# Optimization experiments

Hardware: AMD Instinct MI355X
Metric: run time of the kernel (lower is better)

## Reference

```python
import jax, jax.numpy as jnp
import numpy as np

B, N, D = 1, 2048, 512        # batch, query seq len, model dim
H, DH = 8, 64                 # heads, head dim
MEM = 512                     # cached XL memory tokens (one window segment)
KV = N + MEM                  # kv sequence length
WINDOW = 512                  # block / sliding-window size
LOOKBACK = 1                  # lookback_blocks
N_EP = 4                      # number of episodes
SCALE = DH ** -0.5


def _rope(t, pos):
    # t: [b,h,l,dh], pos: [l]  (GPT-NeoX half rotation)
    dh = t.shape[-1]
    inv_freq = 1.0 / (10000.0 ** (jnp.arange(0, dh, 2, dtype=jnp.float32) / dh))
    freqs = pos.astype(jnp.float32)[:, None] * inv_freq[None, :]   # [l, dh/2]
    freqs = jnp.concatenate([freqs, freqs], axis=-1)               # [l, dh]
    cos, sin = jnp.cos(freqs), jnp.sin(freqs)
    x1, x2 = jnp.split(t, 2, axis=-1)
    rotated = jnp.concatenate([-x2, x1], axis=-1)
    return t * cos + rotated * sin


def setup_inputs() -> dict:
    key = jax.random.key(0)
    ks = jax.random.split(key, 8)
    x = jax.random.normal(ks[0], (B, N, D), jnp.float32)
    cache_k = jax.random.normal(ks[1], (B, H, MEM, DH), jnp.float32)
    cache_v = jax.random.normal(ks[2], (B, H, MEM, DH), jnp.float32)
    episode_ids = jnp.sort(jax.random.randint(ks[3], (B, KV), 0, N_EP, dtype=jnp.int32), axis=-1)
    Wq = jax.random.normal(ks[4], (D, H * DH), jnp.float32) * 0.02
    Wkv = jax.random.normal(ks[5], (D, 2 * H * DH), jnp.float32) * 0.02
    Wg = jax.random.normal(ks[6], (D, H), jnp.float32) * 0.02
    Wo = jax.random.normal(ks[7], (H * DH, D), jnp.float32) * 0.02
    return dict(x=x, cache_k=cache_k, cache_v=cache_v, episode_ids=episode_ids,
                Wq=Wq, Wkv=Wkv, Wg=Wg, Wo=Wo)


def _xl_mask(episode_ids):
    # mirrors create_xl_mask: causal + block window with lookback + intra-episode
    offset = KV - N
    q_pos = offset + jnp.arange(N)          # [N]
    k_pos = jnp.arange(KV)                  # [KV]
    causal = q_pos[:, None] >= k_pos[None, :]
    bq = q_pos // WINDOW
    bk = k_pos // WINDOW
    block = (bq[:, None] >= bk[None, :]) & (bq[:, None] <= bk[None, :] + LOOKBACK)
    intra_ep = episode_ids[:, q_pos][:, :, None] == episode_ids[:, None, :]  # [B,N,KV]
    return (causal & block)[None] & intra_ep                                 # [B,N,KV]


def reference(x, cache_k, cache_v, episode_ids, Wq, Wkv, Wg, Wo):
    b, n, _ = x.shape
    offset = KV - N

    q = (x @ Wq).reshape(b, n, H, DH).transpose(0, 2, 1, 3)          # [b,h,n,dh]
    kv = (x @ Wkv).reshape(b, n, 2, H, DH)
    k_new = kv[:, :, 0].transpose(0, 2, 1, 3)                        # [b,h,n,dh]
    v_new = kv[:, :, 1].transpose(0, 2, 1, 3)

    k = jnp.concatenate([cache_k, k_new], axis=2)                    # [b,h,kv,dh]
    v = jnp.concatenate([cache_v, v_new], axis=2)

    q = _rope(q, offset + jnp.arange(n))
    k = _rope(k, jnp.arange(KV))

    scores = jnp.einsum('bhnd,bhmd->bhnm', q, k) * SCALE             # [b,h,n,kv]
    mask = _xl_mask(episode_ids)[:, None]                            # [b,1,n,kv]
    scores = jnp.where(mask, scores, jnp.finfo(scores.dtype).min)
    attn = jax.nn.softmax(scores, axis=-1)

    out = jnp.einsum('bhnm,bhmd->bhnd', attn, v)                     # [b,h,n,dh]

    gates = jax.nn.sigmoid(x @ Wg).transpose(0, 2, 1)[..., None]     # [b,h,n,1]
    out = out * gates

    out = out.transpose(0, 2, 1, 3).reshape(b, n, H * DH)            # merge heads
    return out @ Wo                                                  # [b,n,d]
```

## Files before the change

kernel.cpp:

```cpp
#include <hip/hip_runtime.h>
#include <math.h>

#define NQ     2048
#define DMODEL 512
#define NH     8
#define DHD    64
#define MEMT   512
#define KVT    2560
#define QSCALE 0.125f
#define NEGF   (-1e30f)

typedef unsigned short u16;
typedef __bf16 bf16x8 __attribute__((ext_vector_type(8)));
typedef float  f32x4  __attribute__((ext_vector_type(4)));
typedef u16    u16x8  __attribute__((ext_vector_type(8)));
typedef u16    u16x4  __attribute__((ext_vector_type(4)));

__device__ __forceinline__ u16 f2bf(float f) {
    union { float f; unsigned u; } v; v.f = f;
    unsigned r = (v.u + 0x7FFFu + ((v.u >> 16) & 1u)) >> 16;
    return (u16)r;
}

__global__ __launch_bounds__(256) void prep(const float* __restrict__ x,
                                            const float* __restrict__ Wq,
                                            const float* __restrict__ Wkv,
                                            const float* __restrict__ Wo,
                                            u16* __restrict__ xb,
                                            u16* __restrict__ Wt,
                                            u16* __restrict__ Wot) {
    __shared__ float tile[64][65];
    int bx = blockIdx.x, tid = threadIdx.x;
    if (bx < 64) {
        int base4 = bx * 4096;
#pragma unroll
        for (int u = 0; u < 16; ++u) {
            int i4 = base4 + u * 256 + tid;
            float4 v = ((const float4*)x)[i4];
            u16x4 o = { f2bf(v.x), f2bf(v.y), f2bf(v.z), f2bf(v.w) };
            *(u16x4*)&xb[i4 * 4] = o;
        }
        return;
    }
    int tt = bx - 64;
    bool isQKV = (tt < 192);
    int tc, tr;
    if (isQKV) { tc = tt % 24; tr = tt / 24; }
    else       { tt -= 192; tc = tt & 7; tr = tt >> 3; }

    int rr = tid >> 4, c4 = (tid & 15) * 4;
#pragma unroll
    for (int u = 0; u < 4; ++u) {
        int row = u * 16 + rr;
        int k = tr * 64 + row;
        int c = tc * 64 + c4;
        float4 v;
        if (isQKV) v = (c < 512) ? *(const float4*)&Wq[k * 512 + c]
                                 : *(const float4*)&Wkv[k * 1024 + (c - 512)];
        else       v = *(const float4*)&Wo[k * 512 + c];
        tile[row][c4 + 0] = v.x; tile[row][c4 + 1] = v.y;
        tile[row][c4 + 2] = v.z; tile[row][c4 + 3] = v.w;
    }
    __syncthreads();
#pragma unroll
    for (int u = 0; u < 4; ++u) {
        int trow = u * 16 + rr;
        u16x4 o;
#pragma unroll
        for (int i = 0; i < 4; ++i) o[i] = f2bf(tile[c4 + i][trow]);
        int t_glob = tc * 64 + trow;
        int k_glob = tr * 64 + c4;
        if (isQKV) *(u16x4*)&Wt[t_glob * 512 + k_glob] = o;
        else       *(u16x4*)&Wot[t_glob * 512 + k_glob] = o;
    }
}

__global__ __launch_bounds__(256) void gates_kernel(const float* __restrict__ x,
                                                    const float* __restrict__ Wg,
                                                    float* __restrict__ gates) {
    int t = blockIdx.x * 256 + threadIdx.x;
    int n = t >> 3, h = t & 7;
    float acc = 0.f;
    for (int k = 0; k < DMODEL; k += 4) {
        float4 xv = *(const float4*)&x[n * DMODEL + k];
        acc += xv.x * Wg[(k + 0) * NH + h] + xv.y * Wg[(k + 1) * NH + h]
             + xv.z * Wg[(k + 2) * NH + h] + xv.w * Wg[(k + 3) * NH + h];
    }
    gates[h * NQ + n] = 1.f / (1.f + expf(-acc));
}

__global__ __launch_bounds__(256) void cache_k_rope(const float* __restrict__ cache_k,
                                                    u16* __restrict__ kb) {
    int h = blockIdx.y, r0 = blockIdx.x * 64;
    int tid = threadIdx.x;
#pragma unroll
    for (int u = 0; u < 8; ++u) {
        int idx = u * 256 + tid;
        int row = idx >> 5, j = idx & 31;
        int r = r0 + row;
        float a = cache_k[(h * MEMT + r) * DHD + j];
        float b = cache_k[(h * MEMT + r) * DHD + 32 + j];
        float invf = powf(10000.f, -(float)j * (1.f / 32.f));
        float ss, sc;
        sincosf((float)r * invf, &ss, &sc);
        kb[(h * KVT + r) * DHD + j]      = f2bf(a * sc - b * ss);
        kb[(h * KVT + r) * DHD + 32 + j] = f2bf(b * sc + a * ss);
    }
}

__global__ __launch_bounds__(256) void v_transpose(const float* __restrict__ cache_v,
                                                   const u16* __restrict__ vn,
                                                   u16* __restrict__ vt) {
    __shared__ u16 tile[64][66];
    int h = blockIdx.y, bx = blockIdx.x;
    int tid = threadIdx.x;
    int rr = tid >> 4, c4 = (tid & 15) * 4;
    if (bx < 8) {
        int r0 = bx * 64;
#pragma unroll
        for (int u = 0; u < 4; ++u) {
            int row = u * 16 + rr;
            float4 v = *(const float4*)&cache_v[(h * MEMT + r0 + row) * DHD + c4];
            tile[row][c4 + 0] = f2bf(v.x); tile[row][c4 + 1] = f2bf(v.y);
            tile[row][c4 + 2] = f2bf(v.z); tile[row][c4 + 3] = f2bf(v.w);
        }
    } else {
        int n0 = (bx - 8) * 64;
#pragma unroll
        for (int u = 0; u < 4; ++u) {
            int row = u * 16 + rr;
            u16x4 v = *(const u16x4*)&vn[(h * NQ + n0 + row) * DHD + c4];
            tile[row][c4 + 0] = v[0]; tile[row][c4 + 1] = v[1];
            tile[row][c4 + 2] = v[2]; tile[row][c4 + 3] = v[3];
        }
    }
    __syncthreads();
    int kvbase = bx * 64;
#pragma unroll
    for (int u = 0; u < 4; ++u) {
        int d = u * 16 + rr;
        u16x4 o = { tile[c4 + 0][d], tile[c4 + 1][d], tile[c4 + 2][d], tile[c4 + 3][d] };
        *(u16x4*)&vt[(h * DHD + d) * KVT + kvbase + c4] = o;
    }
}

template<int MODE>
__global__ __launch_bounds__(256) void gemm_mfma(const u16* __restrict__ A,
                                                 const u16* __restrict__ Bt,
                                                 u16* __restrict__ o_q,
                                                 u16* __restrict__ o_k,
                                                 u16* __restrict__ o_v,
                                                 float* __restrict__ o_f) {
    int bx = blockIdx.x, by = blockIdx.y;
    int tid = threadIdx.x;
    int w = tid >> 6, lane = tid & 63;
    int lr = lane & 15, lg = lane >> 4;
    int rowbase = by * 64 + (w >> 1) * 32;
    int colbase = bx * 64 + (w & 1) * 16;

    f32x4 acc[2][2];
#pragma unroll
    for (int i = 0; i < 2; ++i)
#pragma unroll
        for (int j = 0; j < 2; ++j) { f32x4 z = {0.f, 0.f, 0.f, 0.f}; acc[i][j] = z; }

    const u16* a0 = A + (rowbase + lr) * 512 + lg * 8;
    const u16* a1 = a0 + 16 * 512;
    const u16* b0 = Bt + (colbase + lr) * 512 + lg * 8;
    const u16* b1 = b0 + 32 * 512;

#pragma unroll 4
    for (int k0 = 0; k0 < 512; k0 += 32) {
        bf16x8 fa0 = __builtin_bit_cast(bf16x8, *(const u16x8*)(a0 + k0));
        bf16x8 fa1 = __builtin_bit_cast(bf16x8, *(const u16x8*)(a1 + k0));
        bf16x8 fb0 = __builtin_bit_cast(bf16x8, *(const u16x8*)(b0 + k0));
        bf16x8 fb1 = __builtin_bit_cast(bf16x8, *(const u16x8*)(b1 + k0));
        acc[0][0] = __builtin_amdgcn_mfma_f32_16x16x32_bf16(fa0, fb0, acc[0][0], 0, 0, 0);
        acc[0][1] = __builtin_amdgcn_mfma_f32_16x16x32_bf16(fa0, fb1, acc[0][1], 0, 0, 0);
        acc[1][0] = __builtin_amdgcn_mfma_f32_16x16x32_bf16(fa1, fb0, acc[1][0], 0, 0, 0);
        acc[1][1] = __builtin_amdgcn_mfma_f32_16x16x32_bf16(fa1, fb1, acc[1][1], 0, 0, 0);
    }

    if (MODE == 1) {
#pragma unroll
        for (int rt = 0; rt < 2; ++rt)
#pragma unroll
            for (int r = 0; r < 4; ++r) {
                int n = rowbase + rt * 16 + lg * 4 + r;
                o_f[n * DMODEL + colbase + lr]      = acc[rt][0][r];
                o_f[n * DMODEL + colbase + 32 + lr] = acc[rt][1][r];
            }
        return;
    }

    int j = (colbase & 63) + lr;
    int region = bx >> 3;
    int h = bx & 7;
    float invf = powf(10000.f, -(float)j * (1.f / 32.f));
#pragma unroll
    for (int rt = 0; rt < 2; ++rt)
#pragma unroll
        for (int r = 0; r < 4; ++r) {
            int n = rowbase + rt * 16 + lg * 4 + r;
            float a = acc[rt][0][r], b = acc[rt][1][r];
            if (region == 2) {
                o_v[(h * NQ + n) * DHD + j]      = f2bf(a);
                o_v[(h * NQ + n) * DHD + 32 + j] = f2bf(b);
            } else {
                float ss, sc;
                sincosf((float)(512 + n) * invf, &ss, &sc);
                u16 e0 = f2bf(a * sc - b * ss);
                u16 e1 = f2bf(b * sc + a * ss);
                if (region == 0) {
                    o_q[(h * NQ + n) * DHD + j]      = e0;
                    o_q[(h * NQ + n) * DHD + 32 + j] = e1;
                } else {
                    o_k[(h * KVT + 512 + n) * DHD + j]      = e0;
                    o_k[(h * KVT + 512 + n) * DHD + 32 + j] = e1;
                }
            }
        }
}

#define LOADK(BK, BEP, C0)                                                     \
  _Pragma("unroll")                                                            \
  for (int t = 0; t < 4; ++t) {                                                \
    const u16* kr = kb + ((h * KVT + (C0) + t * 16 + lr) * DHD + lg * 8);      \
    BK[t][0] = __builtin_bit_cast(bf16x8, *(const u16x8*)kr);                  \
    BK[t][1] = __builtin_bit_cast(bf16x8, *(const u16x8*)(kr + 32));           \
    BEP[t] = ep[(C0) + t * 16 + lr];                                           \
  }

#define DO_CHUNK(C0, BK, BEP, PREF, NBK, NBEP)                                 \
  {                                                                            \
    bf16x8 bV[4][2];                                                           \
    _Pragma("unroll")                                                          \
    for (int t = 0; t < 4; ++t) {                                              \
      const u16* vr = vtb + ((h * DHD + t * 16 + lr) * KVT + (C0) + lg * 8);   \
      bV[t][0] = __builtin_bit_cast(bf16x8, *(const u16x8*)vr);                \
      bV[t][1] = __builtin_bit_cast(bf16x8, *(const u16x8*)(vr + 32));         \
    }                                                                          \
    f32x4 s[4];                                                                \
    _Pragma("unroll")                                                          \
    for (int t = 0; t < 4; ++t) {                                              \
      f32x4 z = {0.f, 0.f, 0.f, 0.f};                                          \
      s[t] = __builtin_amdgcn_mfma_f32_16x16x32_bf16(aQ[0], BK[t][0], z, 0, 0, 0); \
      s[t] = __builtin_amdgcn_mfma_f32_16x16x32_bf16(aQ[1], BK[t][1], s[t], 0, 0, 0); \
    }                                                                          \
    if (PREF) { LOADK(NBK, NBEP, (C0) + 64) }                                  \
    float rmax[4] = {NEGF, NEGF, NEGF, NEGF};                                  \
    _Pragma("unroll")                                                          \
    for (int t = 0; t < 4; ++t) {                                              \
      int key = (C0) + t * 16 + lr;                                            \
      int ek = BEP[t];                                                         \
      _Pragma("unroll")                                                        \
      for (int r = 0; r < 4; ++r) {                                            \
        bool vld = (key <= qpos[r]) && (ek == epq[r]);                         \
        float sv = vld ? s[t][r] * QSCALE : NEGF;                              \
        s[t][r] = sv;                                                          \
        rmax[r] = fmaxf(rmax[r], sv);                                          \
      }                                                                        \
    }                                                                          \
    _Pragma("unroll")                                                          \
    for (int mm = 1; mm < 16; mm <<= 1) {                                      \
      _Pragma("unroll")                                                        \
      for (int r = 0; r < 4; ++r)                                              \
        rmax[r] = fmaxf(rmax[r], __shfl_xor(rmax[r], mm, 64));                 \
    }                                                                          \
    float alpha[4];                                                            \
    _Pragma("unroll")                                                          \
    for (int r = 0; r < 4; ++r) {                                              \
      float mn = fmaxf(mrun[r], rmax[r]);                                      \
      alpha[r] = __expf(mrun[r] - mn);                                         \
      mrun[r] = mn;                                                            \
      lsum[r] *= alpha[r];                                                     \
    }                                                                          \
    _Pragma("unroll")                                                          \
    for (int t = 0; t < 4; ++t)                                                \
      _Pragma("unroll")                                                        \
      for (int r = 0; r < 4; ++r) o[t][r] *= alpha[r];                         \
    float psum[4] = {0.f, 0.f, 0.f, 0.f};                                      \
    _Pragma("unroll")                                                          \
    for (int t = 0; t < 4; ++t) {                                              \
      _Pragma("unroll")                                                        \
      for (int r = 0; r < 4; ++r) {                                            \
        float sv = s[t][r];                                                    \
        float p = (sv <= -1e29f) ? 0.f : __expf(sv - mrun[r]);                 \
        psum[r] += p;                                                          \
        int qq = lg * 4 + r;                                                   \
        int kk2 = t * 16 + lr;                                                 \
        pl[qq * 64 + (kk2 ^ ((qq & 7) << 3))] = f2bf(p);                       \
      }                                                                        \
    }                                                                          \
    _Pragma("unroll")                                                          \
    for (int mm = 1; mm < 16; mm <<= 1) {                                      \
      _Pragma("unroll")                                                        \
      for (int r = 0; r < 4; ++r) psum[r] += __shfl_xor(psum[r], mm, 64);      \
    }                                                                          \
    _Pragma("unroll")                                                          \
    for (int r = 0; r < 4; ++r) lsum[r] += psum[r];                            \
    bf16x8 aP[2];                                                              \
    {                                                                          \
      int sw = (lr & 7) << 3;                                                  \
      aP[0] = __builtin_bit_cast(bf16x8, *(const u16x8*)&pl[lr * 64 + ((lg * 8) ^ sw)]);        \
      aP[1] = __builtin_bit_cast(bf16x8, *(const u16x8*)&pl[lr * 64 + ((32 + lg * 8) ^ sw)]);   \
    }                                                                          \
    _Pragma("unroll")                                                          \
    for (int t = 0; t < 4; ++t) {                                              \
      o[t] = __builtin_amdgcn_mfma_f32_16x16x32_bf16(aP[0], bV[t][0], o[t], 0, 0, 0); \
      o[t] = __builtin_amdgcn_mfma_f32_16x16x32_bf16(aP[1], bV[t][1], o[t], 0, 0, 0); \
    }                                                                          \
  }

__global__ __launch_bounds__(256, 1) void attn_mfma(const u16* __restrict__ qb,
                                                    const u16* __restrict__ kb,
                                                    const u16* __restrict__ vtb,
                                                    const float* __restrict__ gates,
                                                    const int* __restrict__ ep,
                                                    u16* __restrict__ outp) {
    __shared__ u16 plds[4][16 * 64];
    int h = blockIdx.y;
    int q0 = blockIdx.x * 64;
    int tid = threadIdx.x;
    int w = tid >> 6, lane = tid & 63;
    int lr = lane & 15, lg = lane >> 4;
    int qbase = q0 + w * 16;
    u16* pl = plds[w];

    bf16x8 aQ[2];
    {
        const u16* qrow = qb + ((h * NQ + qbase + lr) * DHD + lg * 8);
        aQ[0] = __builtin_bit_cast(bf16x8, *(const u16x8*)qrow);
        aQ[1] = __builtin_bit_cast(bf16x8, *(const u16x8*)(qrow + 32));
    }

    int qpos[4], epq[4];
    float gq[4];
#pragma unroll
    for (int r = 0; r < 4; ++r) {
        int q = qbase + lg * 4 + r;
        qpos[r] = 512 + q;
        epq[r] = ep[512 + q];
        gq[r] = gates[h * NQ + q];
    }

    f32x4 o[4];
    float mrun[4], lsum[4];
#pragma unroll
    for (int t = 0; t < 4; ++t) { f32x4 z = {0.f,0.f,0.f,0.f}; o[t] = z; }
#pragma unroll
    for (int r = 0; r < 4; ++r) { mrun[r] = NEGF; lsum[r] = 0.f; }

    int c_lo = q0 & ~511;
    int nch = 9 + ((q0 >> 6) & 7);

    bf16x8 bKA[4][2], bKB[4][2];
    int epA[4], epB[4];

    LOADK(bKA, epA, c_lo)
    int c0 = c_lo, ci = 0;
    while (true) {
        bool more = (ci + 1 < nch);
        DO_CHUNK(c0, bKA, epA, more, bKB, epB)
        ++ci; c0 += 64;
        if (!more) break;
        bool more2 = (ci + 1 < nch);
        DO_CHUNK(c0, bKB, epB, more2, bKA, epA)
        ++ci; c0 += 64;
        if (!more2) break;
    }

#pragma unroll
    for (int r = 0; r < 4; ++r) {
        float inv = gq[r] / lsum[r];
        int q = qbase + lg * 4 + r;
#pragma unroll
        for (int t = 0; t < 4; ++t)
            outp[q * DMODEL + h * DHD + t * 16 + lr] = f2bf(o[t][r] * inv);
    }
}

extern "C" void kernel_launch(void* const* d_in, const int* in_sizes, int n_in,
                              void* d_out, int out_size, void* d_ws, size_t ws_size,
                              hipStream_t stream) {
    const float* x       = (const float*)d_in[0];
    const float* cache_k = (const float*)d_in[1];
    const float* cache_v = (const float*)d_in[2];
    const int*   ep      = (const int*)  d_in[3];
    const float* Wq      = (const float*)d_in[4];
    const float* Wkv     = (const float*)d_in[5];
    const float* Wg      = (const float*)d_in[6];
    const float* Wo      = (const float*)d_in[7];
    float* out = (float*)d_out;

    u16* u = (u16*)d_ws;
    u16* x_bf    = u;
    u16* Wt      = x_bf + 1048576;
    u16* Wot     = Wt + 786432;
    u16* q_bf    = Wot + 262144;
    u16* k_bf    = q_bf + 1048576;
    u16* vn_bf   = k_bf + 1310720;
    u16* vT      = vn_bf + 1048576;
    u16* attn_bf = vT + 1310720;
    float* gatesw = (float*)(attn_bf + 1048576);

    prep<<<320, 256, 0, stream>>>(x, Wq, Wkv, Wo, x_bf, Wt, Wot);
    gates_kernel<<<64, 256, 0, stream>>>(x, Wg, gatesw);
    cache_k_rope<<<dim3(8, 8), 256, 0, stream>>>(cache_k, k_bf);
    gemm_mfma<0><<<dim3(24, 32), 256, 0, stream>>>(x_bf, Wt, q_bf, k_bf, vn_bf, nullptr);
    v_transpose<<<dim3(40, 8), 256, 0, stream>>>(cache_v, vn_bf, vT);
    attn_mfma<<<dim3(32, 8), 256, 0, stream>>>(q_bf, k_bf, vT, gatesw, ep, attn_bf);
    gemm_mfma<1><<<dim3(8, 32), 256, 0, stream>>>(attn_bf, Wot, nullptr, nullptr, nullptr, out);
}
```

Baseline: 158.5 us.

## Split attention KV range across warps, fuse prep kernels, precompute RoPE table

The attention kernel now handles 32 queries per block, with two warp pairs each covering half of the KV chunks. Their partial softmax states are merged through shared memory, which doubles the grid and raises occupancy to 2 blocks per CU. Gates and a sin/cos RoPE table are computed inside the prep kernel, and cache-K rope is folded into the V-transpose kernel, cutting the launch count from 7 to 5. The RoPE table replaces repeated powf/sincosf calls in the GEMM epilogue, at the cost of extra memory reads and a shared-memory merge step.

```diff
diff --git a/kernel.cpp b/kernel.cpp
--- a/kernel.cpp
+++ b/kernel.cpp
@@ -26,11 +26,36 @@
                                             const float* __restrict__ Wq,
                                             const float* __restrict__ Wkv,
                                             const float* __restrict__ Wo,
+                                            const float* __restrict__ Wg,
                                             u16* __restrict__ xb,
                                             u16* __restrict__ Wt,
-                                            u16* __restrict__ Wot) {
+                                            u16* __restrict__ Wot,
+                                            float* __restrict__ gates,
+                                            float2* __restrict__ cs) {
     __shared__ float tile[64][65];
     int bx = blockIdx.x, tid = threadIdx.x;
+
+    if (bx >= 384) {
+        int t = (bx - 384) * 256 + tid;
+        int pos = t >> 5, j = t & 31;
+        float invf = exp2f(-(float)j * (13.287712379549449f / 32.f));
+        float ss, sc;
+        sincosf((float)pos * invf, &ss, &sc);
+        cs[t] = make_float2(sc, ss);
+        return;
+    }
+    if (bx >= 320) {
+        int t = (bx - 320) * 256 + tid;
+        int n = t >> 3, hh = t & 7;
+        float acc = 0.f;
+        for (int k = 0; k < DMODEL; k += 4) {
+            float4 xv = *(const float4*)&x[n * DMODEL + k];
+            acc += xv.x * Wg[(k + 0) * NH + hh] + xv.y * Wg[(k + 1) * NH + hh]
+                 + xv.z * Wg[(k + 2) * NH + hh] + xv.w * Wg[(k + 3) * NH + hh];
+        }
+        gates[hh * NQ + n] = 1.f / (1.f + __expf(-acc));
+        return;
+    }
     if (bx < 64) {
         int base4 = bx * 4096;
 #pragma unroll
@@ -75,48 +100,36 @@
     }
 }
 
-__global__ __launch_bounds__(256) void gates_kernel(const float* __restrict__ x,
-                                                    const float* __restrict__ Wg,
-                                                    float* __restrict__ gates) {
-    int t = blockIdx.x * 256 + threadIdx.x;
-    int n = t >> 3, h = t & 7;
-    float acc = 0.f;
-    for (int k = 0; k < DMODEL; k += 4) {
-        float4 xv = *(const float4*)&x[n * DMODEL + k];
-        acc += xv.x * Wg[(k + 0) * NH + h] + xv.y * Wg[(k + 1) * NH + h]
-             + xv.z * Wg[(k + 2) * NH + h] + xv.w * Wg[(k + 3) * NH + h];
-    }
-    gates[h * NQ + n] = 1.f / (1.f + expf(-acc));
-}
-
-__global__ __launch_bounds__(256) void cache_k_rope(const float* __restrict__ cache_k,
-                                                    u16* __restrict__ kb) {
-    int h = blockIdx.y, r0 = blockIdx.x * 64;
-    int tid = threadIdx.x;
-#pragma unroll
-    for (int u = 0; u < 8; ++u) {
-        int idx = u * 256 + tid;
-        int row = idx >> 5, j = idx & 31;
-        int r = r0 + row;
-        float a = cache_k[(h * MEMT + r) * DHD + j];
-        float b = cache_k[(h * MEMT + r) * DHD + 32 + j];
-        float invf = powf(10000.f, -(float)j * (1.f / 32.f));
-        float ss, sc;
-        sincosf((float)r * invf, &ss, &sc);
-        kb[(h * KVT + r) * DHD + j]      = f2bf(a * sc - b * ss);
-        kb[(h * KVT + r) * DHD + 32 + j] = f2bf(b * sc + a * ss);
-    }
-}
-
-__global__ __launch_bounds__(256) void v_transpose(const float* __restrict__ cache_v,
-                                                   const u16* __restrict__ vn,
-                                                   u16* __restrict__ vt) {
+__global__ __launch_bounds__(256) void kv_prep(const float* __restrict__ cache_k,
+                                               const float* __restrict__ cache_v,
+                                               const u16* __restrict__ vn,
+                                               const float2* __restrict__ cs,
+                                               u16* __restrict__ kb,
+                                               u16* __restrict__ vt) {
     __shared__ u16 tile[64][66];
     int h = blockIdx.y, bx = blockIdx.x;
     int tid = threadIdx.x;
-    int rr = tid >> 4, c4 = (tid & 15) * 4;
+
     if (bx < 8) {
         int r0 = bx * 64;
+#pragma unroll
+        for (int u = 0; u < 8; ++u) {
+            int idx = u * 256 + tid;
+            int row = idx >> 5, j = idx & 31;
+            int r = r0 + row;
+            float a = cache_k[(h * MEMT + r) * DHD + j];
+            float b = cache_k[(h * MEMT + r) * DHD + 32 + j];
+            float2 csv = cs[r * 32 + j];
+            kb[(h * KVT + r) * DHD + j]      = f2bf(a * csv.x - b * csv.y);
+            kb[(h * KVT + r) * DHD + 32 + j] = f2bf(b * csv.x + a * csv.y);
+        }
+        return;
+    }
+
+    int tb = bx - 8;
+    int rr = tid >> 4, c4 = (tid & 15) * 4;
+    if (tb < 8) {
+        int r0 = tb * 64;
 #pragma unroll
         for (int u = 0; u < 4; ++u) {
             int row = u * 16 + rr;
@@ -125,7 +138,7 @@
             tile[row][c4 + 2] = f2bf(v.z); tile[row][c4 + 3] = f2bf(v.w);
         }
     } else {
-        int n0 = (bx - 8) * 64;
+        int n0 = (tb - 8) * 64;
 #pragma unroll
         for (int u = 0; u < 4; ++u) {
             int row = u * 16 + rr;
@@ -135,7 +148,7 @@
         }
     }
     __syncthreads();
-    int kvbase = bx * 64;
+    int kvbase = tb * 64;
 #pragma unroll
     for (int u = 0; u < 4; ++u) {
         int d = u * 16 + rr;
@@ -147,6 +160,7 @@
 template<int MODE>
 __global__ __launch_bounds__(256) void gemm_mfma(const u16* __restrict__ A,
                                                  const u16* __restrict__ Bt,
+                                                 const float2* __restrict__ cs,
                                                  u16* __restrict__ o_q,
                                                  u16* __restrict__ o_k,
                                                  u16* __restrict__ o_v,
@@ -196,7 +210,6 @@
     int j = (colbase & 63) + lr;
     int region = bx >> 3;
     int h = bx & 7;
-    float invf = powf(10000.f, -(float)j * (1.f / 32.f));
 #pragma unroll
     for (int rt = 0; rt < 2; ++rt)
 #pragma unroll
@@ -207,10 +220,9 @@
                 o_v[(h * NQ + n) * DHD + j]      = f2bf(a);
                 o_v[(h * NQ + n) * DHD + 32 + j] = f2bf(b);
             } else {
-                float ss, sc;
-                sincosf((float)(512 + n) * invf, &ss, &sc);
-                u16 e0 = f2bf(a * sc - b * ss);
-                u16 e1 = f2bf(b * sc + a * ss);
+                float2 csv = cs[(512 + n) * 32 + j];
+                u16 e0 = f2bf(a * csv.x - b * csv.y);
+                u16 e1 = f2bf(b * csv.x + a * csv.y);
                 if (region == 0) {
                     o_q[(h * NQ + n) * DHD + j]      = e0;
                     o_q[(h * NQ + n) * DHD + 32 + j] = e1;
@@ -312,19 +324,23 @@
     }                                                                          \
   }
 
-__global__ __launch_bounds__(256, 1) void attn_mfma(const u16* __restrict__ qb,
+__global__ __launch_bounds__(256, 2) void attn_mfma(const u16* __restrict__ qb,
                                                     const u16* __restrict__ kb,
                                                     const u16* __restrict__ vtb,
                                                     const float* __restrict__ gates,
                                                     const int* __restrict__ ep,
                                                     u16* __restrict__ outp) {
     __shared__ u16 plds[4][16 * 64];
+    __shared__ float o_l[2][16][68];
+    __shared__ float ml_l[2][2][16];
+
     int h = blockIdx.y;
-    int q0 = blockIdx.x * 64;
+    int q0 = blockIdx.x * 32;
     int tid = threadIdx.x;
     int w = tid >> 6, lane = tid & 63;
     int lr = lane & 15, lg = lane >> 4;
-    int qbase = q0 + w * 16;
+    int qsub = w & 1, kvh = w >> 1;
+    int qbase = q0 + qsub * 16;
     u16* pl = plds[w];
 
     bf16x8 aQ[2];
@@ -352,31 +368,59 @@
     for (int r = 0; r < 4; ++r) { mrun[r] = NEGF; lsum[r] = 0.f; }
 
     int c_lo = q0 & ~511;
-    int nch = 9 + ((q0 >> 6) & 7);
+    int nch = (544 + (q0 & 511) + 63) >> 6;
+    int n0 = nch >> 1;
+    int my_n = kvh ? (nch - n0) : n0;
+    int c0 = c_lo + (kvh ? (n0 << 6) : 0);
 
     bf16x8 bKA[4][2], bKB[4][2];
     int epA[4], epB[4];
 
-    LOADK(bKA, epA, c_lo)
-    int c0 = c_lo, ci = 0;
+    LOADK(bKA, epA, c0)
+    int ci = 0;
     while (true) {
-        bool more = (ci + 1 < nch);
+        bool more = (ci + 1 < my_n);
         DO_CHUNK(c0, bKA, epA, more, bKB, epB)
         ++ci; c0 += 64;
         if (!more) break;
-        bool more2 = (ci + 1 < nch);
+        bool more2 = (ci + 1 < my_n);
         DO_CHUNK(c0, bKB, epB, more2, bKA, epA)
         ++ci; c0 += 64;
         if (!more2) break;
     }
 
-#pragma unroll
-    for (int r = 0; r < 4; ++r) {
-        float inv = gq[r] / lsum[r];
-        int q = qbase + lg * 4 + r;
+    if (kvh == 1) {
+#pragma unroll
+        for (int r = 0; r < 4; ++r) {
+            ml_l[qsub][0][lg * 4 + r] = mrun[r];
+            ml_l[qsub][1][lg * 4 + r] = lsum[r];
+        }
 #pragma unroll
         for (int t = 0; t < 4; ++t)
-            outp[q * DMODEL + h * DHD + t * 16 + lr] = f2bf(o[t][r] * inv);
+#pragma unroll
+            for (int r = 0; r < 4; ++r)
+                o_l[qsub][lg * 4 + r][t * 16 + lr] = o[t][r];
+    }
+    __syncthreads();
+    if (kvh == 0) {
+#pragma unroll
+        for (int r = 0; r < 4; ++r) {
+            int row = lg * 4 + r;
+            float m1 = ml_l[qsub][0][row], l1 = ml_l[qsub][1][row];
+            float m0 = mrun[r], l0 = lsum[r];
+            float mm2 = fmaxf(m0, m1);
+            float f0 = (m0 <= -1e29f) ? 0.f : __expf(m0 - mm2);
+            float f1 = (m1 <= -1e29f) ? 0.f : __expf(m1 - mm2);
+            float lt = l0 * f0 + l1 * f1;
+            float inv = gq[r] / lt;
+            int q = qbase + row;
+#pragma unroll
+            for (int t = 0; t < 4; ++t) {
+                float o1 = o_l[qsub][row][t * 16 + lr];
+                outp[q * DMODEL + h * DHD + t * 16 + lr] =
+                    f2bf((o[t][r] * f0 + o1 * f1) * inv);
+            }
+        }
     }
 }
 
@@ -402,13 +446,12 @@
     u16* vn_bf   = k_bf + 1310720;
     u16* vT      = vn_bf + 1048576;
     u16* attn_bf = vT + 1310720;
-    float* gatesw = (float*)(attn_bf + 1048576);
-
-    prep<<<320, 256, 0, stream>>>(x, Wq, Wkv, Wo, x_bf, Wt, Wot);
-    gates_kernel<<<64, 256, 0, stream>>>(x, Wg, gatesw);
-    cache_k_rope<<<dim3(8, 8), 256, 0, stream>>>(cache_k, k_bf);
-    gemm_mfma<0><<<dim3(24, 32), 256, 0, stream>>>(x_bf, Wt, q_bf, k_bf, vn_bf, nullptr);
-    v_transpose<<<dim3(40, 8), 256, 0, stream>>>(cache_v, vn_bf, vT);
-    attn_mfma<<<dim3(32, 8), 256, 0, stream>>>(q_bf, k_bf, vT, gatesw, ep, attn_bf);
-    gemm_mfma<1><<<dim3(8, 32), 256, 0, stream>>>(attn_bf, Wot, nullptr, nullptr, nullptr, out);
-}
+    float*  gatesw = (float*)(attn_bf + 1048576);
+    float2* cs     = (float2*)(gatesw + 16384);
+
+    prep<<<704, 256, 0, stream>>>(x, Wq, Wkv, Wo, Wg, x_bf, Wt, Wot, gatesw, cs);
+    gemm_mfma<0><<<dim3(24, 32), 256, 0, stream>>>(x_bf, Wt, cs, q_bf, k_bf, vn_bf, nullptr);
+    kv_prep<<<dim3(48, 8), 256, 0, stream>>>(cache_k, cache_v, vn_bf, cs, k_bf, vT);
+    attn_mfma<<<dim3(64, 8), 256, 0, stream>>>(q_bf, k_bf, vT, gatesw, ep, attn_bf);
+    gemm_mfma<1><<<dim3(8, 32), 256, 0, stream>>>(attn_bf, Wot, nullptr, nullptr, nullptr, nullptr, out);
+}
```

New measurement: 154.8 us. 2.4% less time.
